# Optimization experiments

Hardware: AMD Instinct MI355X
Metric: run time of the kernel (lower is better)

The kernel has to match this reference:

```python
import jax, jax.numpy as jnp
import numpy as np

B, N, IN_DIM, HID, K = 32, 512, 1024, 512, 3
ALPHA = 0.2  # leaky_relu negative slope
NEG = -9e15


def setup_inputs() -> dict:
    key = jax.random.key(0)
    ks = jax.random.split(key, 7)
    hidden_states = jax.random.normal(ks[0], (B, N, IN_DIM), jnp.float32)
    adj = (jax.random.uniform(ks[1], (B, 3, N, N)) < 0.05).astype(jnp.float32)
    W_all = jax.random.normal(ks[2], (3, K, IN_DIM, HID), jnp.float32) * 0.02
    a_all = jax.random.normal(ks[3], (3, K, 2 * HID, 1), jnp.float32) * 0.02
    wawa_w = jax.random.normal(ks[4], (HID, 100), jnp.float32) * 0.05
    wawa_b = jnp.zeros((100,), jnp.float32)
    ctx_w = jax.random.normal(ks[5], (100, 1), jnp.float32) * 0.05
    return {"hidden_states": hidden_states, "adj": adj, "W_all": W_all,
            "a_all": a_all, "wawa_w": wawa_w, "wawa_b": wawa_b, "ctx_w": ctx_w}


def _gat(adj_m, x, W, a):
    # e_ij = leaky_relu(cat[h_i, h_j] @ a) == leaky_relu(h_i@a1 + h_j@a2)
    h = jnp.einsum('bnf,fh->bnh', x, W)           # [B,N,HID]
    f1 = jnp.einsum('bnh,ho->bno', h, a[:HID])    # [B,N,1]
    f2 = jnp.einsum('bnh,ho->bno', h, a[HID:])    # [B,N,1]
    e = jax.nn.leaky_relu(f1 + jnp.swapaxes(f2, 1, 2), negative_slope=ALPHA)  # [B,N,N]
    att = jnp.where(adj_m > 0, e, NEG)
    att = jax.nn.softmax(att, axis=2)
    return jnp.einsum('bnm,bmh->bnh', att, h)


def reference(hidden_states, adj, W_all, a_all, wawa_w, wawa_b, ctx_w):
    adj_a, adj_b, adj_c = adj[:, 0], adj[:, 1], adj[:, 2]
    pa, pb, pc = adj_a, adj_b, adj_c  # matmuls(A, k) = A^(k+1)
    hs = []
    for layer in range(K):
        if layer > 0:
            pa = jnp.matmul(pa, adj_a)
            pb = jnp.matmul(pb, adj_b)
            pc = jnp.matmul(pc, adj_c)
        h_layer = (_gat(pa, hidden_states, W_all[0, layer], a_all[0, layer])
                   + _gat(pb, hidden_states, W_all[1, layer], a_all[1, layer])
                   + _gat(pc, hidden_states, W_all[2, layer], a_all[2, layer]))
        hs.append(h_layer)
    # attention-based combination over the K orders
    s = [jnp.einsum('bnc,co->bno', jnp.tanh(jnp.einsum('bnh,hc->bnc', h, wawa_w) + wawa_b), ctx_w)
         for h in hs]                              # each [B,N,1]
    vs = jax.nn.softmax(jnp.concatenate(s, axis=2), axis=2)  # [B,N,K]
    h_stack = jnp.stack(hs, axis=2)                # [B,N,K,HID]
    return jnp.sum(vs[..., None] * h_stack, axis=2)  # [B,N,HID]
```

## Files before the change

kernel.cpp:

```cpp
#include <hip/hip_runtime.h>
#include <hip/hip_bf16.h>

typedef short v8s __attribute__((ext_vector_type(8)));
typedef float v4f __attribute__((ext_vector_type(4)));
typedef unsigned long long u64;

#define ALPHA 0.2f

__device__ inline unsigned short f32_bf16(float x){
    unsigned int u = __float_as_uint(x);
    unsigned int r = (u + 0x7fffu + ((u >> 16) & 1u)) >> 16;
    return (unsigned short)r;
}
__device__ inline float bf16_f32(unsigned short s){
    return __uint_as_float(((unsigned int)s) << 16);
}
__device__ inline v4f mfma16(v8s a, v8s b, v4f c){
    return __builtin_amdgcn_mfma_f32_16x16x32_bf16(a, b, c, 0, 0, 0);
}
__device__ inline void gload16(const unsigned short* g, short* l){
    __builtin_amdgcn_global_load_lds((const __attribute__((address_space(1))) unsigned int*)g,
                                     (__attribute__((address_space(3))) unsigned int*)l,
                                     16, 0, 0);
}


__global__ void k_convert_x(const float* __restrict__ x, v8s* __restrict__ out, int n8){
    int i = blockIdx.x * 256 + threadIdx.x;
    if (i >= n8) return;
    const float4* p = (const float4*)x + (size_t)i * 2;
    float4 a = p[0], b = p[1];
    v8s r;
    r[0] = (short)f32_bf16(a.x); r[1] = (short)f32_bf16(a.y);
    r[2] = (short)f32_bf16(a.z); r[3] = (short)f32_bf16(a.w);
    r[4] = (short)f32_bf16(b.x); r[5] = (short)f32_bf16(b.y);
    r[6] = (short)f32_bf16(b.z); r[7] = (short)f32_bf16(b.w);
    out[i] = r;
}

__global__ void k_transpose_w(const float* __restrict__ W, unsigned short* __restrict__ Wt){
    __shared__ float tile[32][33];
    int g = blockIdx.z, k0 = blockIdx.x * 32, h0 = blockIdx.y * 32;
    int tx = threadIdx.x, ty = threadIdx.y;
    #pragma unroll
    for (int i = 0; i < 4; ++i)
        tile[ty + i*8][tx] = W[((size_t)g*1024 + k0 + ty + i*8)*512 + h0 + tx];
    __syncthreads();
    #pragma unroll
    for (int i = 0; i < 4; ++i){
        int h = ty + i*8;
        Wt[((size_t)g*512 + h0 + h)*1024 + k0 + tx] = f32_bf16(tile[tx][h]);
    }
}

__global__ void k_wawat(const float* __restrict__ w, unsigned short* __restrict__ wt){
    int i = blockIdx.x * 256 + threadIdx.x;
    if (i >= 128 * 512) return;
    int c = i >> 9, k = i & 511;
    wt[i] = (c < 100) ? f32_bf16(w[k*100 + c]) : (unsigned short)0;
}


__global__ void k_bits(const float* __restrict__ adj, u64* __restrict__ bits){
    int row = blockIdx.x;
    int t = row >> 14, b = (row >> 9) & 31, i = row & 511;
    const float* src = adj + (((size_t)b*3 + t)*512 + i)*512;
    int lane = threadIdx.x;
    #pragma unroll
    for (int w = 0; w < 8; ++w){
        u64 word = __ballot(src[w*64 + lane] > 0.5f);
        if (lane == 0) bits[(size_t)row*8 + w] = word;
    }
}

__global__ __launch_bounds__(256) void k_boolmm(const u64* __restrict__ prev,
                                                const u64* __restrict__ base,
                                                u64* __restrict__ out){
    int row = blockIdx.x * 256 + threadIdx.x;
    if (row >= 49152) return;
    int tb = row >> 9;
    const u64* pr = prev + (size_t)row * 8;
    const u64* bb = base + ((size_t)tb << 9) * 8;
    ulonglong2 a0 = {0,0}, a1 = {0,0}, a2 = {0,0}, a3 = {0,0};
    #pragma unroll
    for (int w = 0; w < 8; ++w){
        u64 m = pr[w];
        const u64* bw = bb + (size_t)(w << 6) * 8;
        while (m){
            int k = __builtin_ctzll(m);
            m &= m - 1;
            const ulonglong2* br = (const ulonglong2*)(bw + (size_t)k * 8);
            ulonglong2 b0 = br[0], b1 = br[1], b2 = br[2], b3 = br[3];
            a0.x |= b0.x; a0.y |= b0.y;
            a1.x |= b1.x; a1.y |= b1.y;
            a2.x |= b2.x; a2.y |= b2.y;
            a3.x |= b3.x; a3.y |= b3.y;
        }
    }
    ulonglong2* op = (ulonglong2*)(out + (size_t)row * 8);
    op[0] = a0; op[1] = a1; op[2] = a2; op[3] = a3;
}

__global__ __launch_bounds__(256, 4) void k_gemm_h(
    const unsigned short* __restrict__ Wt, const unsigned short* __restrict__ Xb,
    unsigned short* __restrict__ Ht, int l)
{
    __shared__ __align__(16) short As[128*32];
    __shared__ __align__(16) short Bs[128*32];
    const int bn = blockIdx.x, bm = blockIdx.y, t = blockIdx.z;
    const int g = t*3 + l;
    const int tid = threadIdx.x;
    const int lane = tid & 63, wave = tid >> 6;
    const int wr = wave >> 1, wc = wave & 1;
    const int fr = lane & 15, fq = lane >> 4;
    const int slot = fq ^ (fr & 3) ^ ((fr >> 2) & 3);

    const int srow = tid >> 2, sw = tid & 3;
    const int gw = sw ^ (srow & 3) ^ ((srow >> 2) & 3);
    const unsigned short* Ap = Wt + ((size_t)g*512 + (size_t)bm*128 + srow)*1024 + gw*8;
    const unsigned short* Bp = Xb + ((size_t)bn*128 + srow)*1024 + gw*8;
    short* AsW = As + wave*512;
    short* BsW = Bs + wave*512;

    v4f acc[4][4] = {};

    for (int kt = 0; kt < 32; ++kt){
        const unsigned short* a0 = Ap + kt*32;
        const unsigned short* b0 = Bp + kt*32;
        gload16(a0,           AsW);
        gload16(a0 + 64*1024, AsW + 2048);
        gload16(b0,           BsW);
        gload16(b0 + 64*1024, BsW + 2048);
        __syncthreads();
        v8s af[4], bf[4];
        #pragma unroll
        for (int i = 0; i < 4; ++i) af[i] = *(const v8s*)&As[(wr*64 + i*16 + fr)*32 + slot*8];
        #pragma unroll
        for (int i = 0; i < 4; ++i) bf[i] = *(const v8s*)&Bs[(wc*64 + i*16 + fr)*32 + slot*8];
        #pragma unroll
        for (int i = 0; i < 4; ++i)
            #pragma unroll
            for (int j = 0; j < 4; ++j)
                acc[i][j] = mfma16(af[i], bf[j], acc[i][j]);
        __syncthreads();
    }
    #pragma unroll
    for (int i = 0; i < 4; ++i){
        const int h = bm*128 + wr*64 + i*16 + fq*4;
        #pragma unroll
        for (int j = 0; j < 4; ++j){
            const int mc = bn*128 + wc*64 + j*16 + fr;
            unsigned short* dst = Ht + ((size_t)t*512 + h)*16384 + mc;
            #pragma unroll
            for (int rg = 0; rg < 4; ++rg)
                dst[(size_t)rg*16384] = f32_bf16(acc[i][j][rg]);
        }
    }
}

__global__ __launch_bounds__(256) void k_f1f2(
    const unsigned short* __restrict__ Ht, const float* __restrict__ aall,
    float* __restrict__ f1, float* __restrict__ f2, int l)
{
    __shared__ float red[256][4];
    const int t = blockIdx.y;
    const int ml = threadIdx.x & 63, hq = threadIdx.x >> 6;
    const int m = (blockIdx.x * 64 + ml) * 2;
    const float* a1 = aall + ((size_t)t*3 + l)*1024;
    const float* a2 = a1 + 512;
    const unsigned int* hp = (const unsigned int*)(Ht + (size_t)t*512*16384 + m);
    float s1a = 0.f, s1b = 0.f, s2a = 0.f, s2b = 0.f;
    #pragma unroll 4
    for (int hh = 0; hh < 128; ++hh){
        int h = hq*128 + hh;
        unsigned int pv = hp[(size_t)h*8192];
        float va = bf16_f32((unsigned short)(pv & 0xffffu));
        float vb = bf16_f32((unsigned short)(pv >> 16));
        float c1 = a1[h], c2 = a2[h];
        s1a += va*c1; s2a += va*c2;
        s1b += vb*c1; s2b += vb*c2;
    }
    red[threadIdx.x][0] = s1a; red[threadIdx.x][1] = s1b;
    red[threadIdx.x][2] = s2a; red[threadIdx.x][3] = s2b;
    __syncthreads();
    if (hq == 0){
        #pragma unroll
        for (int j = 1; j < 4; ++j){
            s1a += red[ml + 64*j][0]; s1b += red[ml + 64*j][1];
            s2a += red[ml + 64*j][2]; s2b += red[ml + 64*j][3];
        }
        f1[t*16384 + m]     = s1a;
        f1[t*16384 + m + 1] = s1b;
        f2[t*16384 + m]     = s2a;
        f2[t*16384 + m + 1] = s2b;
    }
}

__device__ inline void softmax_row(int t, int b, int rt, int r, int q,
    const float* __restrict__ f1a, const float* __restrict__ f2a,
    const u64* __restrict__ maskP, float* p)
{
    const float f1v = f1a[t*16384 + b*512 + rt*64 + r];
    const u64 mw = maskP[(((size_t)t*32 + b)*512 + rt*64 + r)*8 + q];
    const float4* f2p = (const float4*)(f2a + t*16384 + b*512 + q*64);
    float sm = 0.f;
    #pragma unroll
    for (int w = 0; w < 16; ++w){
        float4 f4 = f2p[w];
        #pragma unroll
        for (int u2 = 0; u2 < 4; ++u2){
            int u = w*4 + u2;
            float e = f1v + ((const float*)&f4)[u2];
            e = (e >= 0.f) ? e : ALPHA*e;
            float pe = ((mw >> u) & 1ull) ? __expf(e) : 0.f;
            p[u] = pe; sm += pe;
        }
    }
    sm += __shfl_xor(sm, 1);
    sm += __shfl_xor(sm, 2);
    sm += __shfl_xor(sm, 4);
    const float rinv = 1.f / (sm + 1e-30f);
    #pragma unroll
    for (int u = 0; u < 64; ++u) p[u] *= rinv;
}

__device__ inline void store_att(short* __restrict__ attbuf, int r, int q,
                                 const float* p)
{
    #pragma unroll
    for (int j8 = 0; j8 < 8; ++j8){
        v8s pk;
        #pragma unroll
        for (int u = 0; u < 8; ++u) pk[u] = (short)f32_bf16(p[j8*8 + u]);
        const int cs = q*8 + (j8 ^ q);
        *(v8s*)&attbuf[r*520 + cs*8] = pk;
    }
}

__device__ inline void pv_accum(const short* __restrict__ attbuf,
    const unsigned short* __restrict__ Hb, int wave, int fr, int fq, v4f acc[4][4])
{
    #pragma unroll 2
    for (int kk = 0; kk < 16; ++kk){
        v8s af[4], bv[4];
        const int cb = kk*4 + fq;
        const int cs = (cb & 56) | ((cb & 7) ^ ((cb >> 3) & 7));
        #pragma unroll
        for (int i = 0; i < 4; ++i)
            af[i] = *(const v8s*)&attbuf[(i*16 + fr)*520 + cs*8];
        #pragma unroll
        for (int j = 0; j < 4; ++j)
            bv[j] = *(const v8s*)(Hb + (size_t)(wave*64 + j*16 + fr)*16384 + kk*32 + fq*8);
        #pragma unroll
        for (int i = 0; i < 4; ++i)
            #pragma unroll
            for (int j = 0; j < 4; ++j)
                acc[i][j] = mfma16(af[i], bv[j], acc[i][j]);
    }
}

__global__ __launch_bounds__(512, 2) void k_att_pv(
    const unsigned short* __restrict__ Ht,
    const float* __restrict__ f1a, const float* __restrict__ f2a,
    const u64* __restrict__ maskP,
    unsigned short* __restrict__ hlb)
{
    __shared__ __align__(16) short att0[64*520];
    __shared__ __align__(16) short att1[64*520];
    const int tid = threadIdx.x;
    const int lane = tid & 63, wave = tid >> 6;
    const int b = blockIdx.x, rt = blockIdx.y;
    const int r = tid >> 3, q = tid & 7;
    const int fr = lane & 15, fq = lane >> 4;
    v4f acc[4][4] = {};
    float p[64];

    const unsigned short* Hb0 = Ht + (size_t)b*512;

    softmax_row(0, b, rt, r, q, f1a, f2a, maskP, p);
    store_att(att0, r, q, p);
    __syncthreads();

    softmax_row(1, b, rt, r, q, f1a, f2a, maskP, p);
    store_att(att1, r, q, p);
    pv_accum(att0, Hb0, wave, fr, fq, acc);
    __syncthreads();

    softmax_row(2, b, rt, r, q, f1a, f2a, maskP, p);
    store_att(att0, r, q, p);
    pv_accum(att1, Hb0 + (size_t)512*16384, wave, fr, fq, acc);
    __syncthreads();

    pv_accum(att0, Hb0 + (size_t)2*512*16384, wave, fr, fq, acc);

    #pragma unroll
    for (int i = 0; i < 4; ++i){
        const int row = rt*64 + i*16 + fq*4;
        #pragma unroll
        for (int j = 0; j < 4; ++j){
            const int col = wave*64 + j*16 + fr;
            unsigned short* d1 = hlb + ((size_t)b*512 + row)*512 + col;
            #pragma unroll
            for (int rg = 0; rg < 4; ++rg)
                d1[(size_t)rg*512] = f32_bf16(acc[i][j][rg]);
        }
    }
}

__global__ __launch_bounds__(256) void k_gemm_s(
    const unsigned short* __restrict__ Hb, const unsigned short* __restrict__ Wwt,
    float* __restrict__ C1)
{
    __shared__ __align__(16) short As[128*32];
    __shared__ __align__(16) short Bs[128*32];
    const int bm = blockIdx.x;
    const int tid = threadIdx.x;
    const int lane = tid & 63, wave = tid >> 6;
    const int wr = wave >> 1, wc = wave & 1;
    const int fr = lane & 15, fq = lane >> 4;
    const int slot = fq ^ (fr & 3) ^ ((fr >> 2) & 3);
    const int srow = tid >> 2, sw = tid & 3;
    const int gw = sw ^ (srow & 3) ^ ((srow >> 2) & 3);
    const unsigned short* Ap = Hb + ((size_t)bm*128 + srow)*512 + gw*8;
    const unsigned short* Bp = Wwt + (size_t)srow*512 + gw*8;

    v4f acc[4][4] = {};
    v8s ra0 = *(const v8s*)(Ap);
    v8s ra1 = *(const v8s*)(Ap + 64*512);
    v8s rb0 = *(const v8s*)(Bp);
    v8s rb1 = *(const v8s*)(Bp + 64*512);

    for (int kt = 0; kt < 16; ++kt){
        __syncthreads();
        *(v8s*)&As[tid*8]        = ra0;
        *(v8s*)&As[tid*8 + 2048] = ra1;
        *(v8s*)&Bs[tid*8]        = rb0;
        *(v8s*)&Bs[tid*8 + 2048] = rb1;
        __syncthreads();
        if (kt + 1 < 16){
            const unsigned short* An = Ap + (kt+1)*32;
            const unsigned short* Bn = Bp + (kt+1)*32;
            ra0 = *(const v8s*)(An); ra1 = *(const v8s*)(An + 64*512);
            rb0 = *(const v8s*)(Bn); rb1 = *(const v8s*)(Bn + 64*512);
        }
        v8s af[4], bf[4];
        #pragma unroll
        for (int i = 0; i < 4; ++i) af[i] = *(const v8s*)&As[(wr*64 + i*16 + fr)*32 + slot*8];
        #pragma unroll
        for (int i = 0; i < 4; ++i) bf[i] = *(const v8s*)&Bs[(wc*64 + i*16 + fr)*32 + slot*8];
        #pragma unroll
        for (int i = 0; i < 4; ++i)
            #pragma unroll
            for (int j = 0; j < 4; ++j)
                acc[i][j] = mfma16(af[i], bf[j], acc[i][j]);
    }
    #pragma unroll
    for (int i = 0; i < 4; ++i)
        #pragma unroll
        for (int j = 0; j < 4; ++j)
            #pragma unroll
            for (int rg = 0; rg < 4; ++rg)
                C1[((size_t)bm*128 + wr*64 + i*16 + fq*4 + rg)*128 + wc*64 + j*16 + fr]
                    = acc[i][j][rg];
}

__global__ void k_sv(const float* __restrict__ C1, const float* __restrict__ wb,
                     const float* __restrict__ cw, float* __restrict__ v)
{
    int m = blockIdx.x * 256 + threadIdx.x;
    if (m >= 16384) return;
    float s[3];
    #pragma unroll
    for (int l = 0; l < 3; ++l){
        const float* row = C1 + ((size_t)l*16384 + m)*128;
        float a = 0.f;
        for (int c = 0; c < 100; ++c){
            float x = row[c] + wb[c];
            float th;
            if (x > 15.f) th = 1.f;
            else if (x < -15.f) th = -1.f;
            else { float ex = __expf(2.f*x); th = (ex - 1.f) / (ex + 1.f); }
            a += th * cw[c];
        }
        s[l] = a;
    }
    float m0 = fmaxf(s[0], fmaxf(s[1], s[2]));
    float e0 = __expf(s[0]-m0), e1 = __expf(s[1]-m0), e2 = __expf(s[2]-m0);
    float inv = 1.f / (e0 + e1 + e2);
    v[m] = e0*inv; v[16384 + m] = e1*inv; v[32768 + m] = e2*inv;
}

__global__ void k_comb(const unsigned short* __restrict__ hlb, const float* __restrict__ v,
                       float* __restrict__ out)
{
    int idx = blockIdx.x * 256 + threadIdx.x;
    if (idx >= 16384*64) return;
    int m = idx >> 6, c8 = (idx & 63) << 3;
    const unsigned short* hp = hlb + (size_t)m*512 + c8;
    v8s a = *(const v8s*)hp;
    v8s bb = *(const v8s*)(hp + (size_t)16384*512);
    v8s cc = *(const v8s*)(hp + (size_t)2*16384*512);
    float v0 = v[m], v1 = v[16384+m], v2 = v[32768+m];
    float o[8];
    #pragma unroll
    for (int u = 0; u < 8; ++u)
        o[u] = v0*bf16_f32((unsigned short)a[u])
             + v1*bf16_f32((unsigned short)bb[u])
             + v2*bf16_f32((unsigned short)cc[u]);
    float4* dst = (float4*)(out + (size_t)m*512 + c8);
    dst[0] = make_float4(o[0], o[1], o[2], o[3]);
    dst[1] = make_float4(o[4], o[5], o[6], o[7]);
}

extern "C" void kernel_launch(void* const* d_in, const int* in_sizes, int n_in,
                              void* d_out, int out_size, void* d_ws, size_t ws_size,
                              hipStream_t stream)
{
    (void)in_sizes; (void)n_in; (void)out_size; (void)ws_size;
    const float* hs   = (const float*)d_in[0];
    const float* adj  = (const float*)d_in[1];
    const float* W    = (const float*)d_in[2];
    const float* aall = (const float*)d_in[3];
    const float* ww   = (const float*)d_in[4];
    const float* wb   = (const float*)d_in[5];
    const float* cw   = (const float*)d_in[6];
    float* out = (float*)d_out;
    char* ws = (char*)d_ws;

    unsigned short* Xb  = (unsigned short*)(ws);
    unsigned short* Wt  = (unsigned short*)(ws + 33554432);
    unsigned short* Wwt = (unsigned short*)(ws + 42991616);
    u64* bits           = (u64*)(ws + 43122688);
    u64* P2             = (u64*)(ws + 46268416);
    u64* P3             = (u64*)(ws + 49414144);
    unsigned short* Ht  = (unsigned short*)(ws + 52559872);
    float* f1           = (float*)(ws + 102891520);
    float* f2           = (float*)(ws + 103088128);
    unsigned short* hlb = (unsigned short*)(ws + 203948032);
    float* C1           = (float*)(ws + 52559872);
    float* vv           = (float*)(ws + 102891520);

    k_convert_x<<<8192, 256, 0, stream>>>(hs, (v8s*)Xb, 2097152);
    k_transpose_w<<<dim3(32,16,9), dim3(32,8), 0, stream>>>(W, Wt);
    k_wawat<<<256, 256, 0, stream>>>(ww, Wwt);
    k_bits<<<49152, 64, 0, stream>>>(adj, bits);
    k_boolmm<<<192, 256, 0, stream>>>(bits, bits, P2);
    k_boolmm<<<192, 256, 0, stream>>>(bits, P2, P3);

    const u64* masks[3] = {bits, P2, P3};
    for (int l = 0; l < 3; ++l){
        k_gemm_h<<<dim3(128,4,3), 256, 0, stream>>>(Wt, Xb, Ht, l);
        k_f1f2<<<dim3(128,3), 256, 0, stream>>>(Ht, aall, f1, f2, l);
        k_att_pv<<<dim3(32,8), 512, 0, stream>>>(Ht, f1, f2, masks[l],
            hlb + (size_t)l*16384*512);
    }
    k_gemm_s<<<384, 256, 0, stream>>>(hlb, Wwt, C1);
    k_sv<<<64, 256, 0, stream>>>(C1, wb, cw, vv);
    k_comb<<<4096, 256, 0, stream>>>(hlb, vv, out);
}
```

Measured before the change: 624.9 us.

## Split attention-PV over hidden halves, single LDS buffer, prefetch H fragments

k_att_pv now launches twice as many blocks of 256 threads, each covering half of the hidden dimension. Each block recomputes the full softmax for its 64 rows in a single shared buffer with barriers, replacing the previous double-buffered overlap. The PV loop register-double-buffers the global loads of H fragments so the next k-slice loads while the current one runs on MFMA. k_bits is also repacked from 64-thread blocks into 256-thread blocks of four waves. The cost is that softmax work is duplicated across the two hidden halves and softmax no longer overlaps with the MFMA loop.

```diff
diff --git a/kernel.cpp b/kernel.cpp
--- a/kernel.cpp
+++ b/kernel.cpp
@@ -61,11 +61,12 @@
 }
 
 
-__global__ void k_bits(const float* __restrict__ adj, u64* __restrict__ bits){
-    int row = blockIdx.x;
+__global__ __launch_bounds__(256) void k_bits(const float* __restrict__ adj,
+                                              u64* __restrict__ bits){
+    int row = blockIdx.x * 4 + (threadIdx.x >> 6);
     int t = row >> 14, b = (row >> 9) & 31, i = row & 511;
     const float* src = adj + (((size_t)b*3 + t)*512 + i)*512;
-    int lane = threadIdx.x;
+    int lane = threadIdx.x & 63;
     #pragma unroll
     for (int w = 0; w < 8; ++w){
         u64 word = __ballot(src[w*64 + lane] > 0.5f);
@@ -196,109 +197,105 @@
     }
 }
 
-__device__ inline void softmax_row(int t, int b, int rt, int r, int q,
-    const float* __restrict__ f1a, const float* __restrict__ f2a,
-    const u64* __restrict__ maskP, float* p)
-{
-    const float f1v = f1a[t*16384 + b*512 + rt*64 + r];
-    const u64 mw = maskP[(((size_t)t*32 + b)*512 + rt*64 + r)*8 + q];
-    const float4* f2p = (const float4*)(f2a + t*16384 + b*512 + q*64);
-    float sm = 0.f;
-    #pragma unroll
-    for (int w = 0; w < 16; ++w){
-        float4 f4 = f2p[w];
-        #pragma unroll
-        for (int u2 = 0; u2 < 4; ++u2){
-            int u = w*4 + u2;
-            float e = f1v + ((const float*)&f4)[u2];
-            e = (e >= 0.f) ? e : ALPHA*e;
-            float pe = ((mw >> u) & 1ull) ? __expf(e) : 0.f;
-            p[u] = pe; sm += pe;
-        }
-    }
-    sm += __shfl_xor(sm, 1);
-    sm += __shfl_xor(sm, 2);
-    sm += __shfl_xor(sm, 4);
-    const float rinv = 1.f / (sm + 1e-30f);
-    #pragma unroll
-    for (int u = 0; u < 64; ++u) p[u] *= rinv;
-}
-
-__device__ inline void store_att(short* __restrict__ attbuf, int r, int q,
-                                 const float* p)
-{
-    #pragma unroll
-    for (int j8 = 0; j8 < 8; ++j8){
-        v8s pk;
-        #pragma unroll
-        for (int u = 0; u < 8; ++u) pk[u] = (short)f32_bf16(p[j8*8 + u]);
-        const int cs = q*8 + (j8 ^ q);
-        *(v8s*)&attbuf[r*520 + cs*8] = pk;
-    }
-}
-
-__device__ inline void pv_accum(const short* __restrict__ attbuf,
-    const unsigned short* __restrict__ Hb, int wave, int fr, int fq, v4f acc[4][4])
-{
-    #pragma unroll 2
-    for (int kk = 0; kk < 16; ++kk){
-        v8s af[4], bv[4];
-        const int cb = kk*4 + fq;
-        const int cs = (cb & 56) | ((cb & 7) ^ ((cb >> 3) & 7));
-        #pragma unroll
-        for (int i = 0; i < 4; ++i)
-            af[i] = *(const v8s*)&attbuf[(i*16 + fr)*520 + cs*8];
-        #pragma unroll
-        for (int j = 0; j < 4; ++j)
-            bv[j] = *(const v8s*)(Hb + (size_t)(wave*64 + j*16 + fr)*16384 + kk*32 + fq*8);
-        #pragma unroll
-        for (int i = 0; i < 4; ++i)
-            #pragma unroll
-            for (int j = 0; j < 4; ++j)
-                acc[i][j] = mfma16(af[i], bv[j], acc[i][j]);
-    }
-}
-
-__global__ __launch_bounds__(512, 2) void k_att_pv(
+__global__ __launch_bounds__(256, 2) void k_att_pv(
     const unsigned short* __restrict__ Ht,
     const float* __restrict__ f1a, const float* __restrict__ f2a,
     const u64* __restrict__ maskP,
     unsigned short* __restrict__ hlb)
 {
-    __shared__ __align__(16) short att0[64*520];
-    __shared__ __align__(16) short att1[64*520];
+    __shared__ __align__(16) short att[64*520];
     const int tid = threadIdx.x;
     const int lane = tid & 63, wave = tid >> 6;
-    const int b = blockIdx.x, rt = blockIdx.y;
-    const int r = tid >> 3, q = tid & 7;
+    const int b = blockIdx.x, rt = blockIdx.y, bh = blockIdx.z;
+    const int rq = tid >> 3, q = tid & 7;
     const int fr = lane & 15, fq = lane >> 4;
     v4f acc[4][4] = {};
-    float p[64];
-
-    const unsigned short* Hb0 = Ht + (size_t)b*512;
-
-    softmax_row(0, b, rt, r, q, f1a, f2a, maskP, p);
-    store_att(att0, r, q, p);
-    __syncthreads();
-
-    softmax_row(1, b, rt, r, q, f1a, f2a, maskP, p);
-    store_att(att1, r, q, p);
-    pv_accum(att0, Hb0, wave, fr, fq, acc);
-    __syncthreads();
-
-    softmax_row(2, b, rt, r, q, f1a, f2a, maskP, p);
-    store_att(att0, r, q, p);
-    pv_accum(att1, Hb0 + (size_t)512*16384, wave, fr, fq, acc);
-    __syncthreads();
-
-    pv_accum(att0, Hb0 + (size_t)2*512*16384, wave, fr, fq, acc);
-
+
+    for (int t = 0; t < 3; ++t){
+        __syncthreads();
+        #pragma unroll
+        for (int rr = 0; rr < 2; ++rr){
+            const int r = rr*32 + rq;
+            const float f1v = f1a[t*16384 + b*512 + rt*64 + r];
+            const u64 mw = maskP[(((size_t)t*32 + b)*512 + rt*64 + r)*8 + q];
+            const float4* f2p = (const float4*)(f2a + t*16384 + b*512 + q*64);
+            float p[64];
+            float sm = 0.f;
+            #pragma unroll
+            for (int w = 0; w < 16; ++w){
+                float4 f4 = f2p[w];
+                #pragma unroll
+                for (int u2 = 0; u2 < 4; ++u2){
+                    int u = w*4 + u2;
+                    float e = f1v + ((const float*)&f4)[u2];
+                    e = (e >= 0.f) ? e : ALPHA*e;
+                    float pe = ((mw >> u) & 1ull) ? __expf(e) : 0.f;
+                    p[u] = pe; sm += pe;
+                }
+            }
+            sm += __shfl_xor(sm, 1);
+            sm += __shfl_xor(sm, 2);
+            sm += __shfl_xor(sm, 4);
+            const float rinv = 1.f / (sm + 1e-30f);
+            #pragma unroll
+            for (int j8 = 0; j8 < 8; ++j8){
+                v8s pk;
+                #pragma unroll
+                for (int u = 0; u < 8; ++u)
+                    pk[u] = (short)f32_bf16(p[j8*8 + u] * rinv);
+                const int cs = q*8 + (j8 ^ q);
+                *(v8s*)&att[r*520 + cs*8] = pk;
+            }
+        }
+        __syncthreads();
+        const unsigned short* Hb = Ht + (size_t)t*512*16384
+                                 + (size_t)bh*256*16384 + (size_t)b*512;
+        v8s bv0[4], bv1[4];
+        #pragma unroll
+        for (int j = 0; j < 4; ++j)
+            bv0[j] = *(const v8s*)(Hb + (size_t)(wave*64 + j*16 + fr)*16384 + fq*8);
+        #pragma unroll
+        for (int kk = 0; kk < 16; ++kk){
+            if (kk + 1 < 16){
+                if ((kk + 1) & 1){
+                    #pragma unroll
+                    for (int j = 0; j < 4; ++j)
+                        bv1[j] = *(const v8s*)(Hb + (size_t)(wave*64 + j*16 + fr)*16384
+                                               + (kk+1)*32 + fq*8);
+                } else {
+                    #pragma unroll
+                    for (int j = 0; j < 4; ++j)
+                        bv0[j] = *(const v8s*)(Hb + (size_t)(wave*64 + j*16 + fr)*16384
+                                               + (kk+1)*32 + fq*8);
+                }
+            }
+            v8s af[4];
+            const int cb = kk*4 + fq;
+            const int cs = (cb & 56) | ((cb & 7) ^ ((cb >> 3) & 7));
+            #pragma unroll
+            for (int i = 0; i < 4; ++i)
+                af[i] = *(const v8s*)&att[(i*16 + fr)*520 + cs*8];
+            if (kk & 1){
+                #pragma unroll
+                for (int i = 0; i < 4; ++i)
+                    #pragma unroll
+                    for (int j = 0; j < 4; ++j)
+                        acc[i][j] = mfma16(af[i], bv1[j], acc[i][j]);
+            } else {
+                #pragma unroll
+                for (int i = 0; i < 4; ++i)
+                    #pragma unroll
+                    for (int j = 0; j < 4; ++j)
+                        acc[i][j] = mfma16(af[i], bv0[j], acc[i][j]);
+            }
+        }
+    }
     #pragma unroll
     for (int i = 0; i < 4; ++i){
         const int row = rt*64 + i*16 + fq*4;
         #pragma unroll
         for (int j = 0; j < 4; ++j){
-            const int col = wave*64 + j*16 + fr;
+            const int col = bh*256 + wave*64 + j*16 + fr;
             unsigned short* d1 = hlb + ((size_t)b*512 + row)*512 + col;
             #pragma unroll
             for (int rg = 0; rg < 4; ++rg)
@@ -443,7 +440,7 @@
     k_convert_x<<<8192, 256, 0, stream>>>(hs, (v8s*)Xb, 2097152);
     k_transpose_w<<<dim3(32,16,9), dim3(32,8), 0, stream>>>(W, Wt);
     k_wawat<<<256, 256, 0, stream>>>(ww, Wwt);
-    k_bits<<<49152, 64, 0, stream>>>(adj, bits);
+    k_bits<<<12288, 256, 0, stream>>>(adj, bits);
     k_boolmm<<<192, 256, 0, stream>>>(bits, bits, P2);
     k_boolmm<<<192, 256, 0, stream>>>(bits, P2, P3);
 
@@ -451,7 +448,7 @@
     for (int l = 0; l < 3; ++l){
         k_gemm_h<<<dim3(128,4,3), 256, 0, stream>>>(Wt, Xb, Ht, l);
         k_f1f2<<<dim3(128,3), 256, 0, stream>>>(Ht, aall, f1, f2, l);
-        k_att_pv<<<dim3(32,8), 512, 0, stream>>>(Ht, f1, f2, masks[l],
+        k_att_pv<<<dim3(32,8,2), 256, 0, stream>>>(Ht, f1, f2, masks[l],
             hlb + (size_t)l*16384*512);
     }
     k_gemm_s<<<384, 256, 0, stream>>>(hlb, Wwt, C1);
```

Result: slower. 658.8 us (+5.4%).
